# Kernel optimization log

Hardware: AMD Instinct MI355X
Metric: run time of the kernel (lower is better)

The kernel has to match this reference:

```python
import jax, jax.numpy as jnp
import numpy as np


def setup_inputs() -> dict:
    key = jax.random.key(0)
    k1, k2, k3, k4 = jax.random.split(key, 4)
    B, C, H, W = 16, 16, 128, 128
    return {
        "x": jax.random.normal(k1, (B, C, H, W), dtype=jnp.float32),
        "noise": jax.random.normal(k2, (B, C, H, W), dtype=jnp.float32),
        "wg_param": jax.random.normal(k3, (1, C, 1, 1), dtype=jnp.float32),
        "wnoise_param": jax.random.normal(k4, (1, C, 1, 1), dtype=jnp.float32),
    }


def reference(x, noise, wg_param, wnoise_param):
    # x: [B, C, H, W], C = num_experts
    wg = x * wg_param
    wnoise = jax.nn.softplus(x * wnoise_param)
    Hlogits = wg + noise * wnoise  # noisy gate logits

    # Leave-one-out max over the expert axis, computed with a top-2 trick
    # instead of the O(C^2) masked tensor the torch code materializes.
    Ht = jnp.moveaxis(Hlogits, 1, -1)  # [B, H, W, C]
    top2, _ = jax.lax.top_k(Ht, 2)     # [B, H, W, 2]
    m1, m2 = top2[..., 0:1], top2[..., 1:2]
    amax = jnp.argmax(Ht, axis=-1)     # [B, H, W]
    onehot = jax.nn.one_hot(amax, Ht.shape[-1], dtype=jnp.bool_)  # [B,H,W,C]
    # max over j != i: equals global max unless i is the (arg)max, then 2nd max
    max_excl = jnp.where(onehot, m2, m1)           # [B, H, W, C]
    max_excl = jnp.moveaxis(max_excl, -1, 1)       # [B, C, H, W]

    load_loss = jax.lax.erf((wg - max_excl) / wnoise)

    # RouteTop1: hard top-1 mask applied to softmax; straight-through so the
    # mask is a constant w.r.t. gradients (grad = mask * grad_out).
    s = jax.nn.softmax(Hlogits, axis=1)
    mask = jnp.moveaxis(onehot, -1, 1).astype(s.dtype)
    G = s * jax.lax.stop_gradient(mask)
    return G, load_loss
```

## Files before the change

kernel.cpp:

```cpp
#include <hip/hip_runtime.h>
#include <math.h>

#define NC   16
#define HWSZ (128 * 128)
#define NB   16
#define TOT  (NB * NC * HWSZ)

__device__ __forceinline__ float fast_erf(float v) {
    const float ax = fabsf(v);
    const float t  = __fdividef(1.0f, fmaf(0.3275911f, ax, 1.0f));
    float p = fmaf(1.061405429f, t, -1.453152027f);
    p = fmaf(p, t,  1.421413741f);
    p = fmaf(p, t, -0.284496736f);
    p = fmaf(p, t,  0.254829592f);
    p *= t;
    const float e = __expf(-v * v);
    const float r = fmaf(-p, e, 1.0f);
    return copysignf(r, v);
}

__global__ __launch_bounds__(256) void moe_router_kernel(
    const float* __restrict__ x, const float* __restrict__ noise,
    const float* __restrict__ gp, const float* __restrict__ wnp,
    float* __restrict__ out)
{
    const int t  = blockIdx.x * blockDim.x + threadIdx.x;
    const int b  = t >> 14;
    const int hw = t & (HWSZ - 1);
    const size_t base = (size_t)b * (NC * HWSZ) + hw;

    float wg[NC], wn[NC], hl[NC];
    float m1 = -INFINITY, m2 = -INFINITY;
    int   amax = 0;

    #pragma unroll
    for (int c = 0; c < NC; ++c) {
        const float xv = __builtin_nontemporal_load(x     + base + (size_t)c * HWSZ);
        const float nv = __builtin_nontemporal_load(noise + base + (size_t)c * HWSZ);
        const float wgv = xv * gp[c];
        const float z   = xv * wnp[c];
        const float spv = fmaxf(z, 0.0f) + __logf(1.0f + __expf(-fabsf(z)));
        const float h   = __builtin_fmaf(nv, spv, wgv);
        wg[c] = wgv;
        wn[c] = spv;
        hl[c] = h;
        amax = (h > m1) ? c : amax;
        m2   = fmaxf(m2, fminf(m1, h));
        m1   = fmaxf(m1, h);
    }

    float ssum = 0.0f;
    #pragma unroll
    for (int c = 0; c < NC; ++c)
        ssum += __expf(hl[c] - m1);
    const float ginv = __fdividef(1.0f, ssum);

    #pragma unroll
    for (int c = 0; c < NC; ++c) {
        const bool  top = (c == amax);
        const float mex = top ? m2 : m1;
        const float ll  = fast_erf(__fdividef(wg[c] - mex, wn[c]));
        __builtin_nontemporal_store(top ? ginv : 0.0f, out + base + (size_t)c * HWSZ);
        __builtin_nontemporal_store(ll, out + TOT + base + (size_t)c * HWSZ);
    }
}

extern "C" void kernel_launch(void* const* d_in, const int* in_sizes, int n_in,
                              void* d_out, int out_size, void* d_ws, size_t ws_size,
                              hipStream_t stream) {
    const float* x     = (const float*)d_in[0];
    const float* noise = (const float*)d_in[1];
    const float* gp    = (const float*)d_in[2];
    const float* wnp   = (const float*)d_in[3];
    float* out = (float*)d_out;

    const int threads = NB * HWSZ;
    const int block   = 256;
    const int grid    = threads / block;
    moe_router_kernel<<<grid, block, 0, stream>>>(x, noise, gp, wnp, out);
}
```

Baseline: 17.63 us.

## Split expert channels across lane pairs and merge top-2 and softmax via shuffles

Each pixel is now handled by two adjacent lanes, each covering eight of the sixteen experts. Partial max, second max, argmax and softmax sum are merged with xor shuffles using a rescaled log-sum-exp combine. This doubles the thread count and halves per-thread registers to improve latency hiding, and adds an occupancy hint to the launch bounds. Stores switch from nontemporal to regular. The trade-off is that each wavefront access is split across two channel planes, plus some shuffle and merge overhead.

```diff
diff --git a/kernel.cpp b/kernel.cpp
--- a/kernel.cpp
+++ b/kernel.cpp
@@ -2,6 +2,7 @@
 #include <math.h>
 
 #define NC   16
+#define NCH  8
 #define HWSZ (128 * 128)
 #define NB   16
 #define TOT  (NB * NC * HWSZ)
@@ -15,53 +16,76 @@
     p = fmaf(p, t,  0.254829592f);
     p *= t;
     const float e = __expf(-v * v);
-    const float r = fmaf(-p, e, 1.0f);
-    return copysignf(r, v);
+    return copysignf(fmaf(-p, e, 1.0f), v);
 }
 
-__global__ __launch_bounds__(256) void moe_router_kernel(
+__global__ __launch_bounds__(256, 8) void moe_router_kernel(
     const float* __restrict__ x, const float* __restrict__ noise,
     const float* __restrict__ gp, const float* __restrict__ wnp,
     float* __restrict__ out)
 {
-    const int t  = blockIdx.x * blockDim.x + threadIdx.x;
-    const int b  = t >> 14;
-    const int hw = t & (HWSZ - 1);
-    const size_t base = (size_t)b * (NC * HWSZ) + hw;
+    const int tid = blockIdx.x * blockDim.x + threadIdx.x;
+    const int sp  = tid >> 1;
+    const int cg  = tid & 1;
+    const int b   = sp >> 14;
+    const int hw  = sp & (HWSZ - 1);
+    const size_t base = (size_t)b * (NC * HWSZ) + hw + (size_t)(cg * NCH) * HWSZ;
 
-    float wg[NC], wn[NC], hl[NC];
+    float wg[NCH], wn[NCH], hl[NCH];
     float m1 = -INFINITY, m2 = -INFINITY;
     int   amax = 0;
 
     #pragma unroll
-    for (int c = 0; c < NC; ++c) {
+    for (int c = 0; c < NCH; ++c) {
         const float xv = __builtin_nontemporal_load(x     + base + (size_t)c * HWSZ);
         const float nv = __builtin_nontemporal_load(noise + base + (size_t)c * HWSZ);
-        const float wgv = xv * gp[c];
-        const float z   = xv * wnp[c];
+        const int   ac = cg * NCH + c;
+        const float wgv = xv * gp[ac];
+        const float z   = xv * wnp[ac];
         const float spv = fmaxf(z, 0.0f) + __logf(1.0f + __expf(-fabsf(z)));
         const float h   = __builtin_fmaf(nv, spv, wgv);
         wg[c] = wgv;
         wn[c] = spv;
         hl[c] = h;
-        amax = (h > m1) ? c : amax;
+        amax = (h > m1) ? ac : amax;
         m2   = fmaxf(m2, fminf(m1, h));
         m1   = fmaxf(m1, h);
     }
 
     float ssum = 0.0f;
     #pragma unroll
-    for (int c = 0; c < NC; ++c)
+    for (int c = 0; c < NCH; ++c)
         ssum += __expf(hl[c] - m1);
-    const float ginv = __fdividef(1.0f, ssum);
+
+    const float o_m1   = __shfl_xor(m1, 1);
+    const float o_m2   = __shfl_xor(m2, 1);
+    const int   o_amax = __shfl_xor(amax, 1);
+    const float o_sum  = __shfl_xor(ssum, 1);
+
+    const float m1_0 = (cg == 0) ? m1   : o_m1;
+    const float m1_1 = (cg == 0) ? o_m1 : m1;
+    const float m2_0 = (cg == 0) ? m2   : o_m2;
+    const float m2_1 = (cg == 0) ? o_m2 : m2;
+    const int   am_0 = (cg == 0) ? amax : o_amax;
+    const int   am_1 = (cg == 0) ? o_amax : amax;
+    const float ss_0 = (cg == 0) ? ssum : o_sum;
+    const float ss_1 = (cg == 0) ? o_sum : ssum;
+
+    const float gm1  = fmaxf(m1_0, m1_1);
+    const float gm2  = fmaxf(fminf(m1_0, m1_1), fmaxf(m2_0, m2_1));
+    const int   gam  = (m1_0 >= m1_1) ? am_0 : am_1;
+    const float gsum = __builtin_fmaf(ss_0, __expf(m1_0 - gm1),
+                                      ss_1 * __expf(m1_1 - gm1));
+    const float ginv = __fdividef(1.0f, gsum);
 
     #pragma unroll
-    for (int c = 0; c < NC; ++c) {
-        const bool  top = (c == amax);
-        const float mex = top ? m2 : m1;
+    for (int c = 0; c < NCH; ++c) {
+        const int   ac  = cg * NCH + c;
+        const bool  top = (ac == gam);
+        const float mex = top ? gm2 : gm1;
         const float ll  = fast_erf(__fdividef(wg[c] - mex, wn[c]));
-        __builtin_nontemporal_store(top ? ginv : 0.0f, out + base + (size_t)c * HWSZ);
-        __builtin_nontemporal_store(ll, out + TOT + base + (size_t)c * HWSZ);
+        out[base + (size_t)c * HWSZ]       = top ? ginv : 0.0f;
+        out[TOT + base + (size_t)c * HWSZ] = ll;
     }
 }
 
@@ -74,7 +98,7 @@
     const float* wnp   = (const float*)d_in[3];
     float* out = (float*)d_out;
 
-    const int threads = NB * HWSZ;
+    const int threads = NB * HWSZ * 2;
     const int block   = 256;
     const int grid    = threads / block;
     moe_router_kernel<<<grid, block, 0, stream>>>(x, noise, gp, wnp, out);
```

New measurement: 21.20 us. +20.2%, slower.
